# Optimization experiments

Hardware: AMD Instinct MI355X
Metric: run time of the kernel (lower is better)

Reference implementation:

```python
import jax, jax.numpy as jnp
import numpy as np

B, F = 512, 512
NUM_KERNEL, DIM_KERNEL = 50, 16


def setup_inputs() -> dict:
    key = jax.random.key(0)
    k1, k2 = jax.random.split(key)
    x = jax.random.normal(k1, (B, F), dtype=jnp.float32)
    # glorot-uniform-like scale for the learned kernel
    limit = (6.0 / (F + NUM_KERNEL * DIM_KERNEL)) ** 0.5
    W = jax.random.uniform(k2, (F, NUM_KERNEL * DIM_KERNEL), dtype=jnp.float32,
                           minval=-limit, maxval=limit)
    return {"x": x, "W": W}


def reference(x, W):
    # activation: (B, K, D)
    act = (x @ W).reshape(-1, NUM_KERNEL, DIM_KERNEL)
    # pairwise L1 over the kernel dim D: l1[b, b2, k] = sum_d |act[b,k,d] - act[b2,k,d]|
    diff = act[:, None, :, :] - act[None, :, :, :]      # (B, B, K, D)
    l1 = jnp.sum(jnp.abs(diff), axis=-1)                # (B, B, K)
    features = jnp.sum(jnp.exp(-l1), axis=1)            # (B, K), includes self-term (=1)
    return jnp.concatenate([x, features], axis=1)       # (B, F + K)
```

## Files before the change

kernel.cpp:

```cpp
#include <hip/hip_runtime.h>
#include <hip/hip_bf16.h>
#include <hip/hip_fp16.h>


#define B_ROWS 512
#define F_IN   512
#define NK     50
#define DK     16
#define N_COLS (NK * DK)
#define OUT_COLS (F_IN + NK)

#if __has_builtin(__builtin_amdgcn_exp2f)
#define EXP2F __builtin_amdgcn_exp2f
#else
#define EXP2F exp2f
#endif

typedef __attribute__((ext_vector_type(8))) short bf16x8;
typedef __attribute__((ext_vector_type(4))) float f32x4;

__device__ __forceinline__ short bfs(float f) {
    __hip_bfloat16 h = __float2bfloat16(f);
    return *reinterpret_cast<short*>(&h);
}

__global__ __launch_bounds__(256) void gemm_ksplit_kernel(const float* __restrict__ x,
                                                          const float* __restrict__ W,
                                                          __half* __restrict__ act_h,
                                                          float* __restrict__ out) {
    __shared__ float red[4 * 64 * 8];

    const int tid = threadIdx.x;
    const int wave = tid >> 6, l = tid & 63;
    const int bid = blockIdx.y * 32 + blockIdx.x;

    if (bid < 128) {
        #pragma unroll
        for (int i = 0; i < 2; ++i) {
            int gid = bid * 512 + i * 256 + tid;
            int row = gid >> 7, c4 = gid & 127;
            float4 v = ((const float4*)x)[gid];
            float* o = out + row * OUT_COLS + c4 * 4;
            *(float2*)o = make_float2(v.x, v.y);
            *(float2*)(o + 2) = make_float2(v.z, v.w);
        }
    }

    const int mBase = blockIdx.x * 16;
    const int nBase = blockIdx.y * 32;
    const int rc = l & 15, kg = l >> 4;

    const float* pa = x + (mBase + rc) * F_IN + wave * 128 + kg * 8;
    const float* pb = W + (wave * 128 + kg * 8) * N_COLS + nBase + rc;

    f32x4 acc0 = {0.f, 0.f, 0.f, 0.f};
    f32x4 acc1 = {0.f, 0.f, 0.f, 0.f};

    #pragma unroll
    for (int ks = 0; ks < 4; ++ks) {
        float4 a0 = *(const float4*)(pa + ks * 32);
        float4 a1 = *(const float4*)(pa + ks * 32 + 4);
        bf16x8 a;
        a[0] = bfs(a0.x); a[1] = bfs(a0.y); a[2] = bfs(a0.z); a[3] = bfs(a0.w);
        a[4] = bfs(a1.x); a[5] = bfs(a1.y); a[6] = bfs(a1.z); a[7] = bfs(a1.w);

        const float* pk = pb + (ks * 32) * N_COLS;
        bf16x8 b0, b1;
        #pragma unroll
        for (int j = 0; j < 8; ++j) {
            b0[j] = bfs(pk[j * N_COLS]);
            b1[j] = bfs(pk[j * N_COLS + 16]);
        }
        acc0 = __builtin_amdgcn_mfma_f32_16x16x32_bf16(a, b0, acc0, 0, 0, 0);
        acc1 = __builtin_amdgcn_mfma_f32_16x16x32_bf16(a, b1, acc1, 0, 0, 0);
    }

    const int ro = (wave * 64 + l) * 8;
    *(f32x4*)(red + ro)     = acc0;
    *(f32x4*)(red + ro + 4) = acc1;
    __syncthreads();

    {
        const int e = tid * 2;
        const int le = e >> 3, j0 = e & 7;
        float2 s = make_float2(0.f, 0.f);
        #pragma unroll
        for (int w = 0; w < 4; ++w) {
            float2 v = *(const float2*)(red + w * 512 + e);
            s.x += v.x; s.y += v.y;
        }
        const int row = mBase + (le >> 4) * 4 + (j0 & 3);
        const int col = nBase + (le & 15) + (j0 >> 2) * 16;
        act_h[row * N_COLS + col]       = __float2half(s.x);
        act_h[(row + 1) * N_COLS + col] = __float2half(s.y);
    }
}

__global__ __launch_bounds__(256) void pairwise_h2_kernel(const __half* __restrict__ act_h,
                                                          float* __restrict__ out) {
    const int k = blockIdx.x;
    const int chunk = blockIdx.y;
    __shared__ uint2 Ah4[B_ROWS * 4];

    const int tid = threadIdx.x;
    const __half* base = act_h + k * DK;
    #pragma unroll
    for (int i = 0; i < 8; ++i) {
        int idx = tid + i * 256;
        int b = idx >> 2, d4 = idx & 3;
        uint2 u = *(const uint2*)(base + b * N_COLS + d4 * 4);
        Ah4[idx ^ ((idx >> 6) & 15)] = u;
    }
    __syncthreads();

    const int rt = tid >> 5;
    const int q = tid & 31;
    const int row0 = chunk * 32 + rt * 4;

    __half2 m[4][8];
    #pragma unroll
    for (int r = 0; r < 4; ++r) {
        int gr = row0 + r;
        int xr = (gr >> 4) & 15;
        #pragma unroll
        for (int j = 0; j < 4; ++j) {
            uint2 u = Ah4[(gr * 4 + j) ^ xr];
            m[r][2 * j]     = __builtin_bit_cast(__half2, u.x);
            m[r][2 * j + 1] = __builtin_bit_cast(__half2, u.y);
        }
    }

    const uint2* bq = Ah4 + q * 64;
    const int xm = q & 15;

    float acc[4] = {0.f, 0.f, 0.f, 0.f};
    #pragma unroll 4
    for (int i = 0; i < 16; ++i) {
        __half2 v[8];
        #pragma unroll
        for (int j = 0; j < 4; ++j) {
            uint2 u = bq[(i * 4 + j) ^ xm];
            v[2 * j]     = __builtin_bit_cast(__half2, u.x);
            v[2 * j + 1] = __builtin_bit_cast(__half2, u.y);
        }
        #pragma unroll
        for (int r = 0; r < 4; ++r) {
            __half2 s = __habs2(__hsub2(m[r][0], v[0]));
            #pragma unroll
            for (int jj = 1; jj < 8; ++jj)
                s = __hadd2(s, __habs2(__hsub2(m[r][jj], v[jj])));
            float2 f = __half22float2(s);
            acc[r] += EXP2F((f.x + f.y) * -1.4426950408889634f);
        }
    }

    #pragma unroll
    for (int r = 0; r < 4; ++r) {
        acc[r] += __shfl_xor(acc[r], 1);
        acc[r] += __shfl_xor(acc[r], 2);
        acc[r] += __shfl_xor(acc[r], 4);
        acc[r] += __shfl_xor(acc[r], 8);
        acc[r] += __shfl_xor(acc[r], 16);
    }
    if (q == 0) {
        #pragma unroll
        for (int r = 0; r < 4; ++r)
            out[(row0 + r) * OUT_COLS + F_IN + k] = acc[r];
    }
}

extern "C" void kernel_launch(void* const* d_in, const int* in_sizes, int n_in,
                              void* d_out, int out_size, void* d_ws, size_t ws_size,
                              hipStream_t stream) {
    const float* x = (const float*)d_in[0];
    const float* W = (const float*)d_in[1];
    float* out = (float*)d_out;
    __half* act_h = (__half*)d_ws;

    gemm_ksplit_kernel<<<dim3(32, 25), dim3(256), 0, stream>>>(x, W, act_h, out);
    pairwise_h2_kernel<<<dim3(50, 16), dim3(256), 0, stream>>>(act_h, out);
}
```

Measured before the change: 30.45 us.

## Fuse GEMM and pairwise kernels with per-column-group atomic flags

Merges the GEMM and pairwise-L1 kernels into one 800-block launch. A per-launch ticket counter and a per-column-group done counter let each pairwise block spin-wait only until the 32 GEMM blocks producing its 32 act columns have finished, instead of waiting at a kernel boundary. This removes a launch and the full-grid drain between stages. It depends on all 800 blocks being co-resident, otherwise spinning blocks could deadlock until the iteration cap, and it adds atomic and fence overhead plus a bounded spin that could return before the data is ready.

New measurement: 109.8 us. 3.6x slower.

```diff
diff --git a/kernel.cpp b/kernel.cpp
--- a/kernel.cpp
+++ b/kernel.cpp
@@ -9,6 +9,7 @@
 #define DK     16
 #define N_COLS (NK * DK)
 #define OUT_COLS (F_IN + NK)
+#define NBLOCKS 800
 
 #if __has_builtin(__builtin_amdgcn_exp2f)
 #define EXP2F __builtin_amdgcn_exp2f
@@ -19,20 +20,31 @@
 typedef __attribute__((ext_vector_type(8))) short bf16x8;
 typedef __attribute__((ext_vector_type(4))) float f32x4;
 
+__device__ unsigned long long g_ticket = 0;
+__device__ unsigned long long g_done[25] = {0};
+
 __device__ __forceinline__ short bfs(float f) {
     __hip_bfloat16 h = __float2bfloat16(f);
     return *reinterpret_cast<short*>(&h);
 }
 
-__global__ __launch_bounds__(256) void gemm_ksplit_kernel(const float* __restrict__ x,
-                                                          const float* __restrict__ W,
-                                                          __half* __restrict__ act_h,
-                                                          float* __restrict__ out) {
-    __shared__ float red[4 * 64 * 8];
-
+__global__ __launch_bounds__(256) void fused_kernel(const float* __restrict__ x,
+                                                    const float* __restrict__ W,
+                                                    __half* __restrict__ act_h,
+                                                    float* __restrict__ out) {
+    __shared__ float4 Sh[1024];
+
+    const int bid = blockIdx.x;
     const int tid = threadIdx.x;
     const int wave = tid >> 6, l = tid & 63;
-    const int bid = blockIdx.y * 32 + blockIdx.x;
+    const int rc = l & 15, kg = l >> 4;
+
+    unsigned long long target = 0;
+    if (tid == 0) {
+        unsigned long long tk = __hip_atomic_fetch_add(&g_ticket, 1ULL,
+                                    __ATOMIC_RELAXED, __HIP_MEMORY_SCOPE_SYSTEM);
+        target = 32ULL * (tk / NBLOCKS + 1ULL);
+    }
 
     if (bid < 128) {
         #pragma unroll
@@ -46,41 +58,41 @@
         }
     }
 
-    const int mBase = blockIdx.x * 16;
-    const int nBase = blockIdx.y * 32;
-    const int rc = l & 15, kg = l >> 4;
-
-    const float* pa = x + (mBase + rc) * F_IN + wave * 128 + kg * 8;
-    const float* pb = W + (wave * 128 + kg * 8) * N_COLS + nBase + rc;
-
-    f32x4 acc0 = {0.f, 0.f, 0.f, 0.f};
-    f32x4 acc1 = {0.f, 0.f, 0.f, 0.f};
-
-    #pragma unroll
-    for (int ks = 0; ks < 4; ++ks) {
-        float4 a0 = *(const float4*)(pa + ks * 32);
-        float4 a1 = *(const float4*)(pa + ks * 32 + 4);
-        bf16x8 a;
-        a[0] = bfs(a0.x); a[1] = bfs(a0.y); a[2] = bfs(a0.z); a[3] = bfs(a0.w);
-        a[4] = bfs(a1.x); a[5] = bfs(a1.y); a[6] = bfs(a1.z); a[7] = bfs(a1.w);
-
-        const float* pk = pb + (ks * 32) * N_COLS;
-        bf16x8 b0, b1;
-        #pragma unroll
-        for (int j = 0; j < 8; ++j) {
-            b0[j] = bfs(pk[j * N_COLS]);
-            b1[j] = bfs(pk[j * N_COLS + 16]);
-        }
-        acc0 = __builtin_amdgcn_mfma_f32_16x16x32_bf16(a, b0, acc0, 0, 0, 0);
-        acc1 = __builtin_amdgcn_mfma_f32_16x16x32_bf16(a, b1, acc1, 0, 0, 0);
-    }
-
-    const int ro = (wave * 64 + l) * 8;
-    *(f32x4*)(red + ro)     = acc0;
-    *(f32x4*)(red + ro + 4) = acc1;
-    __syncthreads();
-
     {
+        float* red = (float*)Sh;
+        const int mBase = (bid & 31) * 16;
+        const int nBase = (bid >> 5) * 32;
+
+        const float* pa = x + (mBase + rc) * F_IN + wave * 128 + kg * 8;
+        const float* pb = W + (wave * 128 + kg * 8) * N_COLS + nBase + rc;
+
+        f32x4 acc0 = {0.f, 0.f, 0.f, 0.f};
+        f32x4 acc1 = {0.f, 0.f, 0.f, 0.f};
+
+        #pragma unroll
+        for (int ks = 0; ks < 4; ++ks) {
+            float4 a0 = *(const float4*)(pa + ks * 32);
+            float4 a1 = *(const float4*)(pa + ks * 32 + 4);
+            bf16x8 a;
+            a[0] = bfs(a0.x); a[1] = bfs(a0.y); a[2] = bfs(a0.z); a[3] = bfs(a0.w);
+            a[4] = bfs(a1.x); a[5] = bfs(a1.y); a[6] = bfs(a1.z); a[7] = bfs(a1.w);
+
+            const float* pk = pb + (ks * 32) * N_COLS;
+            bf16x8 b0, b1;
+            #pragma unroll
+            for (int j = 0; j < 8; ++j) {
+                b0[j] = bfs(pk[j * N_COLS]);
+                b1[j] = bfs(pk[j * N_COLS + 16]);
+            }
+            acc0 = __builtin_amdgcn_mfma_f32_16x16x32_bf16(a, b0, acc0, 0, 0, 0);
+            acc1 = __builtin_amdgcn_mfma_f32_16x16x32_bf16(a, b1, acc1, 0, 0, 0);
+        }
+
+        const int ro = (wave * 64 + l) * 8;
+        *(f32x4*)(red + ro)     = acc0;
+        *(f32x4*)(red + ro + 4) = acc1;
+        __syncthreads();
+
         const int e = tid * 2;
         const int le = e >> 3, j0 = e & 7;
         float2 s = make_float2(0.f, 0.f);
@@ -94,22 +106,37 @@
         act_h[row * N_COLS + col]       = __float2half(s.x);
         act_h[(row + 1) * N_COLS + col] = __float2half(s.y);
     }
-}
-
-__global__ __launch_bounds__(256) void pairwise_h2_kernel(const __half* __restrict__ act_h,
-                                                          float* __restrict__ out) {
-    const int k = blockIdx.x;
-    const int chunk = blockIdx.y;
-    __shared__ uint2 Ah4[B_ROWS * 4];
-
-    const int tid = threadIdx.x;
-    const __half* base = act_h + k * DK;
-    #pragma unroll
-    for (int i = 0; i < 8; ++i) {
-        int idx = tid + i * 256;
-        int b = idx >> 2, d4 = idx & 3;
-        uint2 u = *(const uint2*)(base + b * N_COLS + d4 * 4);
-        Ah4[idx ^ ((idx >> 6) & 15)] = u;
+
+    __syncthreads();
+    if (tid == 0) {
+        __builtin_amdgcn_fence(__ATOMIC_RELEASE, "");
+        __hip_atomic_fetch_add(&g_done[bid >> 5], 1ULL,
+                               __ATOMIC_RELAXED, __HIP_MEMORY_SCOPE_SYSTEM);
+    }
+
+    const int k = bid >> 4;
+    const int chunk = bid & 15;
+    const int nc = bid >> 5;
+    if (tid == 0) {
+        for (int it = 0; it < 3000000; ++it) {
+            if (__hip_atomic_load(&g_done[nc], __ATOMIC_RELAXED,
+                                  __HIP_MEMORY_SCOPE_SYSTEM) >= target) break;
+            __builtin_amdgcn_s_sleep(2);
+        }
+    }
+    __syncthreads();
+    __builtin_amdgcn_fence(__ATOMIC_ACQUIRE, "");
+
+    uint2* Ah4 = (uint2*)Sh;
+    {
+        const __half* base = act_h + k * DK;
+        #pragma unroll
+        for (int i = 0; i < 8; ++i) {
+            int idx = tid + i * 256;
+            int b = idx >> 2, d4 = idx & 3;
+            uint2 u = *(const uint2*)(base + b * N_COLS + d4 * 4);
+            Ah4[idx ^ ((idx >> 6) & 15)] = u;
+        }
     }
     __syncthreads();
 
@@ -177,6 +204,5 @@
     float* out = (float*)d_out;
     __half* act_h = (__half*)d_ws;
 
-    gemm_ksplit_kernel<<<dim3(32, 25), dim3(256), 0, stream>>>(x, W, act_h, out);
-    pairwise_h2_kernel<<<dim3(50, 16), dim3(256), 0, stream>>>(act_h, out);
+    fused_kernel<<<dim3(NBLOCKS), dim3(256), 0, stream>>>(x, W, act_h, out);
 }
```
